# Kernel optimization log

Measured on AMD Instinct MI355X. Metric: run time of the kernel, lower is better.

## Reference

```python
import jax, jax.numpy as jnp
import numpy as np

B, T, C = 2, 2048, 2048
H = 16
D = C // H  # head_size = 128
ROPE_BASE = 10000.0


def _rope_cos_sin(seq_len, dim, dtype=jnp.float32):
    # torchtune RotaryPositionalEmbeddings: interleaved pair rotation
    inv_freq = 1.0 / (ROPE_BASE ** (jnp.arange(0, dim, 2, dtype=jnp.float32) / dim))  # [D/2]
    ang = jnp.arange(seq_len, dtype=jnp.float32)[:, None] * inv_freq[None, :]  # [T, D/2]
    return jnp.cos(ang).astype(dtype), jnp.sin(ang).astype(dtype)


def _apply_rope(x, cos, sin):
    # x: [B, T, H, D]; rotate interleaved pairs (even, odd)
    x1 = x[..., 0::2]
    x2 = x[..., 1::2]
    c = cos[None, :, None, :]
    s = sin[None, :, None, :]
    out = jnp.stack([x1 * c - x2 * s, x1 * s + x2 * c], axis=-1)  # [B,T,H,D/2,2]
    return out.reshape(x.shape)


def setup_inputs() -> dict:
    key = jax.random.key(0)
    ks = jax.random.split(key, 5)
    scale = 1.0 / np.sqrt(C)
    return {
        "x": jax.random.normal(ks[0], (B, T, C), jnp.float32),
        "W_attn": jax.random.normal(ks[1], (C, 3 * C), jnp.float32) * scale,
        "b_attn": jax.random.normal(ks[2], (3 * C,), jnp.float32) * 0.01,
        "W_proj": jax.random.normal(ks[3], (C, C), jnp.float32) * scale,
        "b_proj": jax.random.normal(ks[4], (C,), jnp.float32) * 0.01,
    }


def reference(x, W_attn, b_attn, W_proj, b_proj):
    b, t, c = x.shape
    qkv = x @ W_attn + b_attn                      # [B,T,3C]
    q, k, v = jnp.split(qkv, 3, axis=-1)
    q = q.reshape(b, t, H, D)
    k = k.reshape(b, t, H, D)
    v = v.reshape(b, t, H, D)
    cos, sin = _rope_cos_sin(t, D, x.dtype)
    q = _apply_rope(q, cos, sin)
    k = _apply_rope(k, cos, sin)
    # [B,H,T,D]
    q = q.transpose(0, 2, 1, 3)
    k = k.transpose(0, 2, 1, 3)
    v = v.transpose(0, 2, 1, 3)
    scores = jnp.einsum("bhqd,bhkd->bhqk", q, k) / jnp.sqrt(jnp.asarray(D, x.dtype))
    causal = jnp.tril(jnp.ones((t, t), dtype=bool))  # [T,T]
    scores = jnp.where(causal[None, None], scores, jnp.asarray(-jnp.inf, scores.dtype))
    probs = jax.nn.softmax(scores, axis=-1)
    out = jnp.einsum("bhqk,bhkd->bhqd", probs, v)  # [B,H,T,D]
    out = out.transpose(0, 2, 1, 3).reshape(b, t, c)
    return out @ W_proj + b_proj
```

## Files before the change

### kernel.cpp

```cpp
#include <hip/hip_runtime.h>
#include <hip/hip_bf16.h>
#include <math.h>

#define B_ 2
#define T_ 2048
#define C_ 2048
#define H_ 16
#define D_ 128
#define M_ (B_ * T_)
#define N3C (3 * C_)

typedef __attribute__((ext_vector_type(8))) short v8s;
typedef __attribute__((ext_vector_type(4))) float v4f;

typedef const __attribute__((address_space(1))) void* gas_t;
typedef __attribute__((address_space(3))) void* las_t;

__device__ __forceinline__ void gl16(const void* g, void* l) {
  __builtin_amdgcn_global_load_lds((gas_t)g, (las_t)l, 16, 0, 0);
}
__device__ __forceinline__ v8s ldv(const unsigned short* p) { return *(const v8s*)p; }

__device__ inline unsigned short f2bf(float f) {
  unsigned u = __builtin_bit_cast(unsigned, f);
  u += 0x7FFFu + ((u >> 16) & 1u);
  return (unsigned short)(u >> 16);
}
__device__ inline float bf2f(unsigned short h) {
  unsigned u = (unsigned)h << 16;
  return __builtin_bit_cast(float, u);
}

__global__ __launch_bounds__(256) void rope_tab(float2* __restrict__ tab) {
  const int i = blockIdx.x * 256 + threadIdx.x;
  const int t = i >> 6;
  const int ip = i & 63;
  const float RC = 13.28771237954945f / 64.0f;
  float inv = exp2f(-(float)ip * RC);
  float s, c;
  sincosf((float)t * inv, &s, &c);
  float2 v; v.x = c; v.y = s;
  tab[i] = v;
}

__global__ __launch_bounds__(256) void split_rows(
    const float* __restrict__ X, unsigned short* __restrict__ XH,
    unsigned short* __restrict__ XL) {
  const long i4 = ((long)blockIdx.x * 256 + threadIdx.x) * 4;
  float4 v = *(const float4*)(X + i4);
  ushort4 hh, ll;
  hh.x = f2bf(v.x); ll.x = f2bf(v.x - bf2f(hh.x));
  hh.y = f2bf(v.y); ll.y = f2bf(v.y - bf2f(hh.y));
  hh.z = f2bf(v.z); ll.z = f2bf(v.z - bf2f(hh.z));
  hh.w = f2bf(v.w); ll.w = f2bf(v.w - bf2f(hh.w));
  *(ushort4*)&XH[i4] = hh;
  *(ushort4*)&XL[i4] = ll;
}

__global__ __launch_bounds__(256) void convert_wT(
    const float* __restrict__ W, unsigned short* __restrict__ WH,
    unsigned short* __restrict__ WL, int K, int N) {
  __shared__ float Ts[64][68];
  const int tid = threadIdx.x;
  const int n0 = blockIdx.x * 64;
  const int k0 = blockIdx.y * 64;
#pragma unroll
  for (int it = 0; it < 4; ++it) {
    int f = it * 256 + tid;
    int r = f >> 4;
    int c4 = (f & 15) * 4;
    float4 v = *(const float4*)(W + (long)(k0 + r) * N + n0 + c4);
    *(float4*)&Ts[r][c4] = v;
  }
  __syncthreads();
#pragma unroll
  for (int it = 0; it < 4; ++it) {
    int f = it * 256 + tid;
    int rn = f >> 4;
    int c4 = (f & 15) * 4;
    float x0 = Ts[c4 + 0][rn];
    float x1 = Ts[c4 + 1][rn];
    float x2 = Ts[c4 + 2][rn];
    float x3 = Ts[c4 + 3][rn];
    ushort4 hh, ll;
    hh.x = f2bf(x0); ll.x = f2bf(x0 - bf2f(hh.x));
    hh.y = f2bf(x1); ll.y = f2bf(x1 - bf2f(hh.y));
    hh.z = f2bf(x2); ll.z = f2bf(x2 - bf2f(hh.z));
    hh.w = f2bf(x3); ll.w = f2bf(x3 - bf2f(hh.w));
    long o = (long)(n0 + rn) * K + k0 + c4;
    *(ushort4*)&WH[o] = hh;
    *(ushort4*)&WL[o] = ll;
  }
}

#define BAR() do { asm volatile("" ::: "memory"); __builtin_amdgcn_s_barrier(); asm volatile("" ::: "memory"); } while (0)

__global__ __launch_bounds__(512, 1) void gemm_proj_2g(
    const unsigned short* __restrict__ AH, const unsigned short* __restrict__ AL,
    const unsigned short* __restrict__ BH, const unsigned short* __restrict__ BL,
    const float* __restrict__ bias, float* __restrict__ C, int K, int N) {
  __shared__ unsigned short smem[2 * 24576];

  const int tid = threadIdx.x;
  const int lane = tid & 63;
  const int w = tid >> 6;
  const int lm = lane & 15;
  const int quad = lane >> 4;

  const int gx = gridDim.x;
  const int lin = blockIdx.y * gx + blockIdx.x;
  const int pid_m = (lin & 7) + ((lin >> 3) / gx) * 8;
  const int pid_n = (lin >> 3) % gx;
  const int bm = pid_m * 256;
  const int bn = pid_n * 128;

  const int wm = (w & 1) * 128;
  const int wn = (w >> 1) * 32;

  const unsigned short* aS[4]; int aD[4];
  {
    const int seg = tid >> 8;
    const int rr = (tid & 255) >> 2;
    const int cc = tid & 3;
#pragma unroll
    for (int j = 0; j < 4; ++j) {
      int row = (j >> 1) * 64 + seg * 128 + rr;
      int pl = j & 1;
      int c = cc ^ ((row >> 1) & 3);
      aS[j] = (pl ? AL : AH) + (size_t)(bm + row) * K + c * 8;
      aD[j] = pl * 8192 + row * 32 + cc * 8;
    }
  }
  const unsigned short* bS[2]; int bD[2];
#pragma unroll
  for (int j = 0; j < 2; ++j) {
    int p = tid;
    int row = p >> 2;
    int c = (p & 3) ^ ((row >> 1) & 3);
    bS[j] = (j ? BL : BH) + (size_t)(bn + row) * K + c * 8;
    bD[j] = 16384 + j * 4096 + p * 8;
  }

  v4f acc[8][2];
#pragma unroll
  for (int i = 0; i < 8; ++i)
#pragma unroll
    for (int j = 0; j < 2; ++j) {
      v4f z = {0.f, 0.f, 0.f, 0.f};
      acc[i][j] = z;
    }

  const int kswz = (quad ^ ((lm >> 1) & 3)) * 8;
  const int nk = K >> 5;

  gl16(bS[0], smem + bD[0]);
  gl16(bS[1], smem + bD[1]);
  gl16(aS[0], smem + aD[0]);
  gl16(aS[1], smem + aD[1]);
  gl16(aS[2], smem + aD[2]);
  gl16(aS[3], smem + aD[3]);

#define MM3(MT, NT, AH_, AL_)                                                           \
  acc[MT][NT] = __builtin_amdgcn_mfma_f32_16x16x32_bf16(AH_, bh##NT, acc[MT][NT], 0, 0, 0); \
  acc[MT][NT] = __builtin_amdgcn_mfma_f32_16x16x32_bf16(AH_, bl##NT, acc[MT][NT], 0, 0, 0); \
  acc[MT][NT] = __builtin_amdgcn_mfma_f32_16x16x32_bf16(AL_, bh##NT, acc[MT][NT], 0, 0, 0);
#define MROW(MT, XH_, XL_) MM3(MT, 0, XH_, XL_) MM3(MT, 1, XH_, XL_)
#define AFRAG(MT) ldv(sbuf + (wm + (MT) * 16 + lm) * 32 + kswz)
#define AFRAGL(MT) ldv(sbuf + 8192 + (wm + (MT) * 16 + lm) * 32 + kswz)

  for (int t = 0; t < nk; ++t) {
    const unsigned short* sbuf = smem + (t & 1) * 24576;
    unsigned short* nbuf = (unsigned short*)smem + ((t + 1) & 1) * 24576;
    const int kn = (t + 1) * 32;
    const bool pf = (t + 1 < nk);

    if (pf) {
      gl16(bS[0] + kn, nbuf + bD[0]);
      gl16(bS[1] + kn, nbuf + bD[1]);
      asm volatile("s_waitcnt vmcnt(4)" ::: "memory");
    } else {
      asm volatile("s_waitcnt vmcnt(2)" ::: "memory");
    }
    BAR();

    v8s bh0 = ldv(sbuf + 16384 + (wn + lm) * 32 + kswz);
    v8s bl0 = ldv(sbuf + 20480 + (wn + lm) * 32 + kswz);
    v8s bh1 = ldv(sbuf + 16384 + (wn + 16 + lm) * 32 + kswz);
    v8s bl1 = ldv(sbuf + 20480 + (wn + 16 + lm) * 32 + kswz);
    {
      v8s x0h = AFRAG(0), x0l = AFRAGL(0);
      v8s x1h = AFRAG(1), x1l = AFRAGL(1);
      v8s x2h = AFRAG(2), x2l = AFRAGL(2);
      v8s x3h = AFRAG(3), x3l = AFRAGL(3);
      __builtin_amdgcn_s_setprio(1);
      MROW(0, x0h, x0l)
      MROW(1, x1h, x1l)
      __builtin_amdgcn_s_setprio(0);
      if (pf) {
        gl16(aS[0] + kn, nbuf + aD[0]);
        gl16(aS[1] + kn, nbuf + aD[1]);
      }
      __builtin_amdgcn_s_setprio(1);
      MROW(2, x2h, x2l)
      MROW(3, x3h, x3l)
      __builtin_amdgcn_s_setprio(0);
    }

    if (pf) {
      gl16(aS[2] + kn, nbuf + aD[2]);
      gl16(aS[3] + kn, nbuf + aD[3]);
      asm volatile("s_waitcnt vmcnt(6)" ::: "memory");
    } else {
      asm volatile("s_waitcnt vmcnt(0)" ::: "memory");
    }
    BAR();

    {
      v8s x4h = AFRAG(4), x4l = AFRAGL(4);
      v8s x5h = AFRAG(5), x5l = AFRAGL(5);
      v8s x6h = AFRAG(6), x6l = AFRAGL(6);
      v8s x7h = AFRAG(7), x7l = AFRAGL(7);
      __builtin_amdgcn_s_setprio(1);
      MROW(4, x4h, x4l)
      MROW(5, x5h, x5l)
      MROW(6, x6h, x6l)
      MROW(7, x7h, x7l)
      __builtin_amdgcn_s_setprio(0);
    }
    BAR();
  }
#undef AFRAGL
#undef AFRAG
#undef MROW
#undef MM3

  __syncthreads();
  float* eps = (float*)smem;
  float* myeps = eps + w * 1088;

  float bv[2];
#pragma unroll
  for (int nt = 0; nt < 2; ++nt) bv[nt] = bias[bn + wn + nt * 16 + lm];

  const int r2 = lane >> 2;
  const int c4 = (lane & 3) * 4;
#pragma unroll
  for (int mt = 0; mt < 8; ++mt) {
#pragma unroll
    for (int nt = 0; nt < 2; ++nt)
#pragma unroll
      for (int r = 0; r < 4; ++r)
        myeps[(quad * 4 + r) * 68 + nt * 16 + lm] = acc[mt][nt][r] + bv[nt];
    float* dst = C + (size_t)(bm + wm + mt * 16 + r2) * N + bn + wn + c4;
#pragma unroll
    for (int i = 0; i < 2; ++i) {
      float4 v = *(float4*)&myeps[r2 * 68 + c4 + i * 16];
      *(float4*)&dst[i * 16] = v;
    }
  }
}

__global__ __launch_bounds__(512, 2) void gemm_qkv_8ph(
    const unsigned short* __restrict__ AH, const unsigned short* __restrict__ AL,
    const unsigned short* __restrict__ BH, const unsigned short* __restrict__ BL,
    const float* __restrict__ bias, const float2* __restrict__ tab,
    unsigned short* __restrict__ QH, unsigned short* __restrict__ QL,
    unsigned short* __restrict__ KH, unsigned short* __restrict__ KL,
    unsigned short* __restrict__ VH, unsigned short* __restrict__ VL,
    int K, int N) {
  __shared__ unsigned short smem[2 * 28672];

  const int tid = threadIdx.x;
  const int lane = tid & 63;
  const int w = tid >> 6;
  const int lm = lane & 15;
  const int quad = lane >> 4;

  const int gx = gridDim.x;
  const int lin = blockIdx.y * gx + blockIdx.x;
  const int pid_m = (lin & 7) + ((lin >> 3) / gx) * 8;
  const int pid_n = (lin >> 3) % gx;
  const int bm = pid_m * 256;
  const int bn = pid_n * 192;

  const int wm = (w & 1) * 128;
  const int wn = (w >> 1) * 48;

  const unsigned short* aS[4]; int aD[4];
  {
    const int seg = tid >> 8;
    const int rr = (tid & 255) >> 2;
    const int cc = tid & 3;
#pragma unroll
    for (int j = 0; j < 4; ++j) {
      int row = (j >> 1) * 64 + seg * 128 + rr;
      int pl = j & 1;
      int c = cc ^ ((row >> 1) & 3);
      aS[j] = (pl ? AL : AH) + (size_t)(bm + row) * K + c * 8;
      aD[j] = pl * 8192 + row * 32 + cc * 8;
    }
  }
  const unsigned short* bS[3]; int bD[3];
#pragma unroll
  for (int j = 0; j < 3; ++j) {
    int g = tid + 512 * j;
    int pl = (g >= 768) ? 1 : 0;
    int p = g - pl * 768;
    int row = p >> 2;
    int c = (p & 3) ^ ((row >> 1) & 3);
    bS[j] = (pl ? BL : BH) + (size_t)(bn + row) * K + c * 8;
    bD[j] = 16384 + pl * 6144 + p * 8;
  }

  v4f acc[8][3];
#pragma unroll
  for (int i = 0; i < 8; ++i)
#pragma unroll
    for (int j = 0; j < 3; ++j) {
      v4f z = {0.f, 0.f, 0.f, 0.f};
      acc[i][j] = z;
    }

  const int kswz = (quad ^ ((lm >> 1) & 3)) * 8;
  const int nk = K >> 5;

  gl16(bS[0], smem + bD[0]);
  gl16(bS[1], smem + bD[1]);
  gl16(bS[2], smem + bD[2]);
  gl16(aS[0], smem + aD[0]);
  gl16(aS[1], smem + aD[1]);
  gl16(aS[2], smem + aD[2]);
  gl16(aS[3], smem + aD[3]);

#define MM3(MT, NT, AH_, AL_)                                                           \
  acc[MT][NT] = __builtin_amdgcn_mfma_f32_16x16x32_bf16(AH_, bh##NT, acc[MT][NT], 0, 0, 0); \
  acc[MT][NT] = __builtin_amdgcn_mfma_f32_16x16x32_bf16(AH_, bl##NT, acc[MT][NT], 0, 0, 0); \
  acc[MT][NT] = __builtin_amdgcn_mfma_f32_16x16x32_bf16(AL_, bh##NT, acc[MT][NT], 0, 0, 0);
#define MROW(MT, XH_, XL_) MM3(MT, 0, XH_, XL_) MM3(MT, 1, XH_, XL_) MM3(MT, 2, XH_, XL_)
#define AFRAG(MT) ldv(sbuf + (wm + (MT) * 16 + lm) * 32 + kswz)
#define AFRAGL(MT) ldv(sbuf + 8192 + (wm + (MT) * 16 + lm) * 32 + kswz)

  for (int t = 0; t < nk; ++t) {
    const unsigned short* sbuf = smem + (t & 1) * 28672;
    unsigned short* nbuf = (unsigned short*)smem + ((t + 1) & 1) * 28672;
    const int kn = (t + 1) * 32;
    const bool pf = (t + 1 < nk);

    if (pf) {
      gl16(bS[0] + kn, nbuf + bD[0]);
      gl16(bS[1] + kn, nbuf + bD[1]);
      gl16(bS[2] + kn, nbuf + bD[2]);
      asm volatile("s_waitcnt vmcnt(5)" ::: "memory");
    } else {
      asm volatile("s_waitcnt vmcnt(2)" ::: "memory");
    }
    BAR();

    v8s bh0 = ldv(sbuf + 16384 + (wn + lm) * 32 + kswz);
    v8s bl0 = ldv(sbuf + 22528 + (wn + lm) * 32 + kswz);
    v8s bh1 = ldv(sbuf + 16384 + (wn + 16 + lm) * 32 + kswz);
    v8s bl1 = ldv(sbuf + 22528 + (wn + 16 + lm) * 32 + kswz);
    v8s bh2 = ldv(sbuf + 16384 + (wn + 32 + lm) * 32 + kswz);
    v8s bl2 = ldv(sbuf + 22528 + (wn + 32 + lm) * 32 + kswz);
    {
      v8s x0h = AFRAG(0), x0l = AFRAGL(0);
      v8s x1h = AFRAG(1), x1l = AFRAGL(1);
      v8s x2h = AFRAG(2), x2l = AFRAGL(2);
      v8s x3h = AFRAG(3), x3l = AFRAGL(3);
      __builtin_amdgcn_s_setprio(1);
      MROW(0, x0h, x0l)
      MROW(1, x1h, x1l)
      __builtin_amdgcn_s_setprio(0);
      if (pf) {
        gl16(aS[0] + kn, nbuf + aD[0]);
        gl16(aS[1] + kn, nbuf + aD[1]);
      }
      __builtin_amdgcn_s_setprio(1);
      MROW(2, x2h, x2l)
      MROW(3, x3h, x3l)
      __builtin_amdgcn_s_setprio(0);
    }

    if (pf) {
      gl16(aS[2] + kn, nbuf + aD[2]);
      gl16(aS[3] + kn, nbuf + aD[3]);
      asm volatile("s_waitcnt vmcnt(7)" ::: "memory");
    } else {
      asm volatile("s_waitcnt vmcnt(0)" ::: "memory");
    }
    BAR();

    {
      v8s x4h = AFRAG(4), x4l = AFRAGL(4);
      v8s x5h = AFRAG(5), x5l = AFRAGL(5);
      v8s x6h = AFRAG(6), x6l = AFRAGL(6);
      v8s x7h = AFRAG(7), x7l = AFRAGL(7);
      __builtin_amdgcn_s_setprio(1);
      MROW(4, x4h, x4l)
      MROW(5, x5h, x5l)
      MROW(6, x6h, x6l)
      MROW(7, x7h, x7l)
      __builtin_amdgcn_s_setprio(0);
    }
    BAR();
  }
#undef AFRAGL
#undef AFRAG
#undef MROW
#undef MM3

  __syncthreads();
  float* eps = (float*)smem;
  float* myeps = eps + w * 1088;

  float bv[3];
#pragma unroll
  for (int nt = 0; nt < 3; ++nt) bv[nt] = bias[bn + wn + nt * 16 + lm];

  const int r2 = lane >> 2;
  const int c4 = (lane & 3) * 4;

#pragma unroll
  for (int mt = 0; mt < 8; ++mt) {
#pragma unroll
    for (int nt = 0; nt < 3; ++nt)
#pragma unroll
      for (int r = 0; r < 4; ++r)
        myeps[(quad * 4 + r) * 68 + nt * 16 + lm] = acc[mt][nt][r] + bv[nt];

    const int row = bm + wm + mt * 16 + r2;
    const int bb = row >> 11;
    const int tt = row & 2047;
#pragma unroll
    for (int i = 0; i < 3; ++i) {
      float4 v = *(float4*)&myeps[r2 * 68 + c4 + i * 16];
      const int col = bn + wn + c4 + i * 16;
      const int part = col >> 11;
      const int cc = col & 2047;
      const int hh = cc >> 7;
      const int d0 = cc & 127;
      size_t dst = ((size_t)(bb * H_ + hh) * T_ + tt) * D_ + d0;
      if (part < 2) {
        const float sc = part ? 1.0f : 0.12751879523595298f;
        const int ip = d0 >> 1;
        float2 t0 = tab[tt * 64 + ip];
        float2 t1 = tab[tt * 64 + ip + 1];
        float ox0 = (v.x * t0.x - v.y * t0.y) * sc;
        float oy0 = (v.x * t0.y + v.y * t0.x) * sc;
        float ox1 = (v.z * t1.x - v.w * t1.y) * sc;
        float oy1 = (v.z * t1.y + v.w * t1.x) * sc;
        unsigned short h0 = f2bf(ox0), h1 = f2bf(oy0);
        unsigned short h2 = f2bf(ox1), h3 = f2bf(oy1);
        ushort4 hv; hv.x = h0; hv.y = h1; hv.z = h2; hv.w = h3;
        ushort4 lv;
        lv.x = f2bf(ox0 - bf2f(h0)); lv.y = f2bf(oy0 - bf2f(h1));
        lv.z = f2bf(ox1 - bf2f(h2)); lv.w = f2bf(oy1 - bf2f(h3));
        unsigned short* OH = part ? KH : QH;
        unsigned short* OL = part ? KL : QL;
        *(ushort4*)&OH[dst] = hv;
        *(ushort4*)&OL[dst] = lv;
      } else {
        unsigned short h0 = f2bf(v.x), h1 = f2bf(v.y);
        unsigned short h2 = f2bf(v.z), h3 = f2bf(v.w);
        ushort4 hv; hv.x = h0; hv.y = h1; hv.z = h2; hv.w = h3;
        ushort4 lv;
        lv.x = f2bf(v.x - bf2f(h0)); lv.y = f2bf(v.y - bf2f(h1));
        lv.z = f2bf(v.z - bf2f(h2)); lv.w = f2bf(v.w - bf2f(h3));
        *(ushort4*)&VH[dst] = hv;
        *(ushort4*)&VL[dst] = lv;
      }
    }
  }
}

__global__ __launch_bounds__(256) void v_trans(
    const unsigned short* __restrict__ VH, const unsigned short* __restrict__ VL,
    unsigned short* __restrict__ VTH, unsigned short* __restrict__ VTL) {
  const int tb = blockIdx.x;
  const int h = blockIdx.y;
  const int b = blockIdx.z;
  const int tid = threadIdx.x;

  __shared__ unsigned short TH[128][66];
  __shared__ unsigned short TL[128][66];

  const size_t base = (size_t)(b * H_ + h) * T_ * D_;
#pragma unroll
  for (int it = 0; it < 4; ++it) {
    int f = it * 256 + tid;
    int r = f >> 4;
    int c8 = (f & 15) * 8;
    uint4 hv = *(const uint4*)&VH[base + (size_t)(tb * 64 + r) * D_ + c8];
    uint4 lv = *(const uint4*)&VL[base + (size_t)(tb * 64 + r) * D_ + c8];
    const unsigned short* hp = (const unsigned short*)&hv;
    const unsigned short* lp = (const unsigned short*)&lv;
#pragma unroll
    for (int j = 0; j < 8; ++j) {
      TH[c8 + j][r] = hp[j];
      TL[c8 + j][r] = lp[j];
    }
  }
  __syncthreads();
  const size_t obase = (size_t)(b * H_ + h) * D_ * T_;
#pragma unroll
  for (int it = 0; it < 4; ++it) {
    int f = it * 256 + tid;
    int d = f >> 3;
    int c8 = (f & 7) * 8;
    unsigned short th[8], tl[8];
#pragma unroll
    for (int j = 0; j < 8; ++j) { th[j] = TH[d][c8 + j]; tl[j] = TL[d][c8 + j]; }
    size_t dst = obase + (size_t)d * T_ + tb * 64 + c8;
    *(uint4*)&VTH[dst] = *(uint4*)th;
    *(uint4*)&VTL[dst] = *(uint4*)tl;
  }
}

__global__ __launch_bounds__(512, 4) void attn_mfma(
    const unsigned short* __restrict__ QH, const unsigned short* __restrict__ QL,
    const unsigned short* __restrict__ KH, const unsigned short* __restrict__ KL,
    const unsigned short* __restrict__ VTH, const unsigned short* __restrict__ VTL,
    unsigned short* __restrict__ OHp, unsigned short* __restrict__ OLp) {
  const int qb = (int)gridDim.x - 1 - (int)blockIdx.x;
  const int h = blockIdx.y;
  const int b = blockIdx.z;
  const int tid = threadIdx.x;
  const int lane = tid & 63;
  const int w = tid >> 6;
  const int lm = lane & 15;
  const int quad = lane >> 4;

  __shared__ unsigned short KS_H[32][136], KS_L[32][136];
  __shared__ unsigned short VS_H[128][40], VS_L[128][40];
  __shared__ unsigned short PS_H[128][40], PS_L[128][40];

  const size_t qbase = ((size_t)(b * H_ + h) * T_ + qb * 128 + w * 16 + lm) * D_;
  v8s qh[4], ql[4];
#pragma unroll
  for (int ks = 0; ks < 4; ++ks) {
    qh[ks] = *(const v8s*)&QH[qbase + ks * 32 + quad * 8];
    ql[ks] = *(const v8s*)&QL[qbase + ks * 32 + quad * 8];
  }

  v8s ones;
#pragma unroll
  for (int j = 0; j < 8; ++j) ones[j] = (short)0x3F80;

  const int kr = tid >> 4;
  const int kc = (tid & 15) * 8;
  const int vd = tid >> 2;
  const int vc = (tid & 3) * 8;

  const size_t kbase0 = (size_t)(b * H_ + h) * T_ * D_;
  const size_t vbase0 = (size_t)(b * H_ + h) * D_ * T_;
  const int nkb = 4 * qb + 4;

  uint4 khp = *(const uint4*)&KH[kbase0 + (size_t)kr * D_ + kc];
  uint4 klp = *(const uint4*)&KL[kbase0 + (size_t)kr * D_ + kc];
  uint4 vhp = *(const uint4*)&VTH[vbase0 + (size_t)vd * T_ + vc];
  uint4 vlp = *(const uint4*)&VTL[vbase0 + (size_t)vd * T_ + vc];

  v4f acc_o[8], acc_l;
#pragma unroll
  for (int nt = 0; nt < 8; ++nt) {
    v4f z = {0.f, 0.f, 0.f, 0.f};
    acc_o[nt] = z;
  }
  {
    v4f z = {0.f, 0.f, 0.f, 0.f};
    acc_l = z;
  }

  const float M2 = 32.0f;

  for (int kb = 0; kb < nkb; ++kb) {
    __syncthreads();
    *(uint4*)&KS_H[kr][kc] = khp;
    *(uint4*)&KS_L[kr][kc] = klp;
    *(uint4*)&VS_H[vd][vc] = vhp;
    *(uint4*)&VS_L[vd][vc] = vlp;
    __syncthreads();

    if (kb + 1 < nkb) {
      size_t kg = kbase0 + (size_t)((kb + 1) * 32 + kr) * D_ + kc;
      khp = *(const uint4*)&KH[kg];
      klp = *(const uint4*)&KL[kg];
      size_t vg = vbase0 + (size_t)vd * T_ + (kb + 1) * 32 + vc;
      vhp = *(const uint4*)&VTH[vg];
      vlp = *(const uint4*)&VTL[vg];
    }

    v4f s0, s1;
    {
      v4f z = {0.f, 0.f, 0.f, 0.f};
      s0 = z; s1 = z;
    }
#pragma unroll
    for (int ks = 0; ks < 4; ++ks) {
      int k8 = ks * 32 + quad * 8;
      v8s bh0 = *(const v8s*)&KS_H[lm][k8];
      v8s bl0 = *(const v8s*)&KS_L[lm][k8];
      v8s bh1 = *(const v8s*)&KS_H[16 + lm][k8];
      v8s bl1 = *(const v8s*)&KS_L[16 + lm][k8];
      s0 = __builtin_amdgcn_mfma_f32_16x16x32_bf16(qh[ks], bh0, s0, 0, 0, 0);
      s1 = __builtin_amdgcn_mfma_f32_16x16x32_bf16(qh[ks], bh1, s1, 0, 0, 0);
      s0 = __builtin_amdgcn_mfma_f32_16x16x32_bf16(qh[ks], bl0, s0, 0, 0, 0);
      s1 = __builtin_amdgcn_mfma_f32_16x16x32_bf16(qh[ks], bl1, s1, 0, 0, 0);
      s0 = __builtin_amdgcn_mfma_f32_16x16x32_bf16(ql[ks], bh0, s0, 0, 0, 0);
      s1 = __builtin_amdgcn_mfma_f32_16x16x32_bf16(ql[ks], bh1, s1, 0, 0, 0);
    }

#pragma unroll
    for (int r = 0; r < 4; ++r) {
      int rowg = qb * 128 + w * 16 + quad * 4 + r;
      float v0 = (kb * 32 + lm > rowg) ? -INFINITY : s0[r];
      float v1 = (kb * 32 + 16 + lm > rowg) ? -INFINITY : s1[r];
      float p0 = __builtin_amdgcn_exp2f(v0 - M2);
      float p1 = __builtin_amdgcn_exp2f(v1 - M2);

      int prow = w * 16 + quad * 4 + r;
      unsigned short p0h = f2bf(p0);
      PS_H[prow][lm] = p0h;
      PS_L[prow][lm] = f2bf(p0 - bf2f(p0h));
      unsigned short p1h = f2bf(p1);
      PS_H[prow][16 + lm] = p1h;
      PS_L[prow][16 + lm] = f2bf(p1 - bf2f(p1h));
    }

    v8s ph = *(const v8s*)&PS_H[w * 16 + lm][quad * 8];
    v8s pl = *(const v8s*)&PS_L[w * 16 + lm][quad * 8];
    acc_l = __builtin_amdgcn_mfma_f32_16x16x32_bf16(ph, ones, acc_l, 0, 0, 0);
    acc_l = __builtin_amdgcn_mfma_f32_16x16x32_bf16(pl, ones, acc_l, 0, 0, 0);
#pragma unroll
    for (int nt = 0; nt < 8; ++nt) {
      v8s vh = *(const v8s*)&VS_H[nt * 16 + lm][quad * 8];
      v8s vl = *(const v8s*)&VS_L[nt * 16 + lm][quad * 8];
      acc_o[nt] = __builtin_amdgcn_mfma_f32_16x16x32_bf16(ph, vh, acc_o[nt], 0, 0, 0);
      acc_o[nt] = __builtin_amdgcn_mfma_f32_16x16x32_bf16(ph, vl, acc_o[nt], 0, 0, 0);
      acc_o[nt] = __builtin_amdgcn_mfma_f32_16x16x32_bf16(pl, vh, acc_o[nt], 0, 0, 0);
    }
  }

#pragma unroll
  for (int r = 0; r < 4; ++r) {
    float invl = 1.0f / acc_l[r];
    size_t row = (size_t)(b * T_ + qb * 128 + w * 16 + quad * 4 + r);
#pragma unroll
    for (int nt = 0; nt < 8; ++nt) {
      float o = acc_o[nt][r] * invl;
      unsigned short oh = f2bf(o);
      size_t idx = row * C_ + h * D_ + nt * 16 + lm;
      OHp[idx] = oh;
      OLp[idx] = f2bf(o - bf2f(oh));
    }
  }
}

extern "C" void kernel_launch(void* const* d_in, const int* in_sizes, int n_in,
                              void* d_out, int out_size, void* d_ws, size_t ws_size,
                              hipStream_t stream) {
  const float* x      = (const float*)d_in[0];
  const float* W_attn = (const float*)d_in[1];
  const float* b_attn = (const float*)d_in[2];
  const float* W_proj = (const float*)d_in[3];
  const float* b_proj = (const float*)d_in[4];
  float* out = (float*)d_out;

  char* wsb = (char*)d_ws;
  const size_t MiB = 1048576;
  unsigned short* XH   = (unsigned short*)(wsb + 0 * MiB);
  unsigned short* XL   = (unsigned short*)(wsb + 16 * MiB);
  unsigned short* WtaH = (unsigned short*)(wsb + 32 * MiB);
  unsigned short* WtaL = (unsigned short*)(wsb + 56 * MiB);
  unsigned short* QH   = (unsigned short*)(wsb + 80 * MiB);
  unsigned short* QL   = (unsigned short*)(wsb + 96 * MiB);
  unsigned short* KH   = (unsigned short*)(wsb + 112 * MiB);
  unsigned short* KL   = (unsigned short*)(wsb + 128 * MiB);
  unsigned short* VH   = (unsigned short*)(wsb + 144 * MiB);
  unsigned short* VL   = (unsigned short*)(wsb + 160 * MiB);
  float2*         tab  = (float2*)(wsb + 176 * MiB);
  unsigned short* VTH  = (unsigned short*)(wsb + 0 * MiB);
  unsigned short* VTL  = (unsigned short*)(wsb + 16 * MiB);
  unsigned short* WtpH = (unsigned short*)(wsb + 32 * MiB);
  unsigned short* WtpL = (unsigned short*)(wsb + 40 * MiB);
  unsigned short* AOH  = (unsigned short*)(wsb + 48 * MiB);
  unsigned short* AOL  = (unsigned short*)(wsb + 64 * MiB);

  rope_tab<<<dim3((T_ * 64) / 256), 256, 0, stream>>>(tab);
  convert_wT<<<dim3(N3C / 64, C_ / 64), 256, 0, stream>>>(W_attn, WtaH, WtaL, C_, N3C);
  split_rows<<<dim3((M_ * C_) / 1024), 256, 0, stream>>>(x, XH, XL);
  gemm_qkv_8ph<<<dim3(N3C / 192, M_ / 256), 512, 0, stream>>>(
      XH, XL, WtaH, WtaL, b_attn, tab, QH, QL, KH, KL, VH, VL, C_, N3C);
  v_trans<<<dim3(T_ / 64, H_, B_), 256, 0, stream>>>(VH, VL, VTH, VTL);
  convert_wT<<<dim3(C_ / 64, C_ / 64), 256, 0, stream>>>(W_proj, WtpH, WtpL, C_, C_);
  attn_mfma<<<dim3(T_ / 128, H_, B_), 512, 0, stream>>>(
      QH, QL, KH, KL, VTH, VTL, AOH, AOL);
  gemm_proj_2g<<<dim3(C_ / 128, M_ / 256), 512, 0, stream>>>(
      AOH, AOL, WtpH, WtpL, b_proj, out, C_, C_);
}
```

Measured before the change: 693.2 us.

## Give each attention wave two query row tiles and halve block threads

The attention kernel now launches 256 threads instead of 512, and each wave computes two 16-row query tiles instead of one. Each K/V fragment read from LDS is reused across both tiles, and every thread stages twice as many K/V elements per step. This cuts LDS read traffic and the number of waves per block, at the cost of more registers per thread (launch bounds drop to 256,2) and so possibly lower occupancy.

```diff
diff --git a/kernel.cpp b/kernel.cpp
--- a/kernel.cpp
+++ b/kernel.cpp
@@ -516,7 +516,7 @@
   }
 }
 
-__global__ __launch_bounds__(512, 4) void attn_mfma(
+__global__ __launch_bounds__(256, 2) void attn_mfma(
     const unsigned short* __restrict__ QH, const unsigned short* __restrict__ QL,
     const unsigned short* __restrict__ KH, const unsigned short* __restrict__ KL,
     const unsigned short* __restrict__ VTH, const unsigned short* __restrict__ VTL,
@@ -534,12 +534,16 @@
   __shared__ unsigned short VS_H[128][40], VS_L[128][40];
   __shared__ unsigned short PS_H[128][40], PS_L[128][40];
 
-  const size_t qbase = ((size_t)(b * H_ + h) * T_ + qb * 128 + w * 16 + lm) * D_;
-  v8s qh[4], ql[4];
-#pragma unroll
-  for (int ks = 0; ks < 4; ++ks) {
-    qh[ks] = *(const v8s*)&QH[qbase + ks * 32 + quad * 8];
-    ql[ks] = *(const v8s*)&QL[qbase + ks * 32 + quad * 8];
+  v8s qh[2][4], ql[2][4];
+#pragma unroll
+  for (int mq = 0; mq < 2; ++mq) {
+    const size_t qbase =
+        ((size_t)(b * H_ + h) * T_ + qb * 128 + w * 32 + mq * 16 + lm) * D_;
+#pragma unroll
+    for (int ks = 0; ks < 4; ++ks) {
+      qh[mq][ks] = *(const v8s*)&QH[qbase + ks * 32 + quad * 8];
+      ql[mq][ks] = *(const v8s*)&QL[qbase + ks * 32 + quad * 8];
+    }
   }
 
   v8s ones;
@@ -555,45 +559,59 @@
   const size_t vbase0 = (size_t)(b * H_ + h) * D_ * T_;
   const int nkb = 4 * qb + 4;
 
-  uint4 khp = *(const uint4*)&KH[kbase0 + (size_t)kr * D_ + kc];
-  uint4 klp = *(const uint4*)&KL[kbase0 + (size_t)kr * D_ + kc];
-  uint4 vhp = *(const uint4*)&VTH[vbase0 + (size_t)vd * T_ + vc];
-  uint4 vlp = *(const uint4*)&VTL[vbase0 + (size_t)vd * T_ + vc];
-
-  v4f acc_o[8], acc_l;
-#pragma unroll
-  for (int nt = 0; nt < 8; ++nt) {
+  uint4 khp0 = *(const uint4*)&KH[kbase0 + (size_t)kr * D_ + kc];
+  uint4 khp1 = *(const uint4*)&KH[kbase0 + (size_t)(kr + 16) * D_ + kc];
+  uint4 klp0 = *(const uint4*)&KL[kbase0 + (size_t)kr * D_ + kc];
+  uint4 klp1 = *(const uint4*)&KL[kbase0 + (size_t)(kr + 16) * D_ + kc];
+  uint4 vhp0 = *(const uint4*)&VTH[vbase0 + (size_t)vd * T_ + vc];
+  uint4 vhp1 = *(const uint4*)&VTH[vbase0 + (size_t)(vd + 64) * T_ + vc];
+  uint4 vlp0 = *(const uint4*)&VTL[vbase0 + (size_t)vd * T_ + vc];
+  uint4 vlp1 = *(const uint4*)&VTL[vbase0 + (size_t)(vd + 64) * T_ + vc];
+
+  v4f acc_o[2][8], acc_l[2];
+#pragma unroll
+  for (int mq = 0; mq < 2; ++mq) {
+#pragma unroll
+    for (int nt = 0; nt < 8; ++nt) {
+      v4f z = {0.f, 0.f, 0.f, 0.f};
+      acc_o[mq][nt] = z;
+    }
     v4f z = {0.f, 0.f, 0.f, 0.f};
-    acc_o[nt] = z;
-  }
-  {
-    v4f z = {0.f, 0.f, 0.f, 0.f};
-    acc_l = z;
+    acc_l[mq] = z;
   }
 
   const float M2 = 32.0f;
 
   for (int kb = 0; kb < nkb; ++kb) {
     __syncthreads();
-    *(uint4*)&KS_H[kr][kc] = khp;
-    *(uint4*)&KS_L[kr][kc] = klp;
-    *(uint4*)&VS_H[vd][vc] = vhp;
-    *(uint4*)&VS_L[vd][vc] = vlp;
+    *(uint4*)&KS_H[kr][kc] = khp0;
+    *(uint4*)&KS_H[kr + 16][kc] = khp1;
+    *(uint4*)&KS_L[kr][kc] = klp0;
+    *(uint4*)&KS_L[kr + 16][kc] = klp1;
+    *(uint4*)&VS_H[vd][vc] = vhp0;
+    *(uint4*)&VS_H[vd + 64][vc] = vhp1;
+    *(uint4*)&VS_L[vd][vc] = vlp0;
+    *(uint4*)&VS_L[vd + 64][vc] = vlp1;
     __syncthreads();
 
     if (kb + 1 < nkb) {
       size_t kg = kbase0 + (size_t)((kb + 1) * 32 + kr) * D_ + kc;
-      khp = *(const uint4*)&KH[kg];
-      klp = *(const uint4*)&KL[kg];
+      khp0 = *(const uint4*)&KH[kg];
+      khp1 = *(const uint4*)&KH[kg + (size_t)16 * D_];
+      klp0 = *(const uint4*)&KL[kg];
+      klp1 = *(const uint4*)&KL[kg + (size_t)16 * D_];
       size_t vg = vbase0 + (size_t)vd * T_ + (kb + 1) * 32 + vc;
-      vhp = *(const uint4*)&VTH[vg];
-      vlp = *(const uint4*)&VTL[vg];
-    }
-
-    v4f s0, s1;
-    {
+      vhp0 = *(const uint4*)&VTH[vg];
+      vhp1 = *(const uint4*)&VTH[vg + (size_t)64 * T_];
+      vlp0 = *(const uint4*)&VTL[vg];
+      vlp1 = *(const uint4*)&VTL[vg + (size_t)64 * T_];
+    }
+
+    v4f s[2][2];
+#pragma unroll
+    for (int mq = 0; mq < 2; ++mq) {
       v4f z = {0.f, 0.f, 0.f, 0.f};
-      s0 = z; s1 = z;
+      s[mq][0] = z; s[mq][1] = z;
     }
 #pragma unroll
     for (int ks = 0; ks < 4; ++ks) {
@@ -602,56 +620,72 @@
       v8s bl0 = *(const v8s*)&KS_L[lm][k8];
       v8s bh1 = *(const v8s*)&KS_H[16 + lm][k8];
       v8s bl1 = *(const v8s*)&KS_L[16 + lm][k8];
-      s0 = __builtin_amdgcn_mfma_f32_16x16x32_bf16(qh[ks], bh0, s0, 0, 0, 0);
-      s1 = __builtin_amdgcn_mfma_f32_16x16x32_bf16(qh[ks], bh1, s1, 0, 0, 0);
-      s0 = __builtin_amdgcn_mfma_f32_16x16x32_bf16(qh[ks], bl0, s0, 0, 0, 0);
-      s1 = __builtin_amdgcn_mfma_f32_16x16x32_bf16(qh[ks], bl1, s1, 0, 0, 0);
-      s0 = __builtin_amdgcn_mfma_f32_16x16x32_bf16(ql[ks], bh0, s0, 0, 0, 0);
-      s1 = __builtin_amdgcn_mfma_f32_16x16x32_bf16(ql[ks], bh1, s1, 0, 0, 0);
-    }
-
-#pragma unroll
-    for (int r = 0; r < 4; ++r) {
-      int rowg = qb * 128 + w * 16 + quad * 4 + r;
-      float v0 = (kb * 32 + lm > rowg) ? -INFINITY : s0[r];
-      float v1 = (kb * 32 + 16 + lm > rowg) ? -INFINITY : s1[r];
-      float p0 = __builtin_amdgcn_exp2f(v0 - M2);
-      float p1 = __builtin_amdgcn_exp2f(v1 - M2);
-
-      int prow = w * 16 + quad * 4 + r;
-      unsigned short p0h = f2bf(p0);
-      PS_H[prow][lm] = p0h;
-      PS_L[prow][lm] = f2bf(p0 - bf2f(p0h));
-      unsigned short p1h = f2bf(p1);
-      PS_H[prow][16 + lm] = p1h;
-      PS_L[prow][16 + lm] = f2bf(p1 - bf2f(p1h));
-    }
-
-    v8s ph = *(const v8s*)&PS_H[w * 16 + lm][quad * 8];
-    v8s pl = *(const v8s*)&PS_L[w * 16 + lm][quad * 8];
-    acc_l = __builtin_amdgcn_mfma_f32_16x16x32_bf16(ph, ones, acc_l, 0, 0, 0);
-    acc_l = __builtin_amdgcn_mfma_f32_16x16x32_bf16(pl, ones, acc_l, 0, 0, 0);
+#pragma unroll
+      for (int mq = 0; mq < 2; ++mq) {
+        s[mq][0] = __builtin_amdgcn_mfma_f32_16x16x32_bf16(qh[mq][ks], bh0, s[mq][0], 0, 0, 0);
+        s[mq][1] = __builtin_amdgcn_mfma_f32_16x16x32_bf16(qh[mq][ks], bh1, s[mq][1], 0, 0, 0);
+        s[mq][0] = __builtin_amdgcn_mfma_f32_16x16x32_bf16(qh[mq][ks], bl0, s[mq][0], 0, 0, 0);
+        s[mq][1] = __builtin_amdgcn_mfma_f32_16x16x32_bf16(qh[mq][ks], bl1, s[mq][1], 0, 0, 0);
+        s[mq][0] = __builtin_amdgcn_mfma_f32_16x16x32_bf16(ql[mq][ks], bh0, s[mq][0], 0, 0, 0);
+        s[mq][1] = __builtin_amdgcn_mfma_f32_16x16x32_bf16(ql[mq][ks], bh1, s[mq][1], 0, 0, 0);
+      }
+    }
+
+#pragma unroll
+    for (int mq = 0; mq < 2; ++mq) {
+#pragma unroll
+      for (int r = 0; r < 4; ++r) {
+        int rowg = qb * 128 + w * 32 + mq * 16 + quad * 4 + r;
+        float v0 = (kb * 32 + lm > rowg) ? -INFINITY : s[mq][0][r];
+        float v1 = (kb * 32 + 16 + lm > rowg) ? -INFINITY : s[mq][1][r];
+        float p0 = __builtin_amdgcn_exp2f(v0 - M2);
+        float p1 = __builtin_amdgcn_exp2f(v1 - M2);
+
+        int prow = w * 32 + mq * 16 + quad * 4 + r;
+        unsigned short p0h = f2bf(p0);
+        PS_H[prow][lm] = p0h;
+        PS_L[prow][lm] = f2bf(p0 - bf2f(p0h));
+        unsigned short p1h = f2bf(p1);
+        PS_H[prow][16 + lm] = p1h;
+        PS_L[prow][16 + lm] = f2bf(p1 - bf2f(p1h));
+      }
+    }
+
+    v8s ph0 = *(const v8s*)&PS_H[w * 32 + lm][quad * 8];
+    v8s pl0 = *(const v8s*)&PS_L[w * 32 + lm][quad * 8];
+    v8s ph1 = *(const v8s*)&PS_H[w * 32 + 16 + lm][quad * 8];
+    v8s pl1 = *(const v8s*)&PS_L[w * 32 + 16 + lm][quad * 8];
+    acc_l[0] = __builtin_amdgcn_mfma_f32_16x16x32_bf16(ph0, ones, acc_l[0], 0, 0, 0);
+    acc_l[0] = __builtin_amdgcn_mfma_f32_16x16x32_bf16(pl0, ones, acc_l[0], 0, 0, 0);
+    acc_l[1] = __builtin_amdgcn_mfma_f32_16x16x32_bf16(ph1, ones, acc_l[1], 0, 0, 0);
+    acc_l[1] = __builtin_amdgcn_mfma_f32_16x16x32_bf16(pl1, ones, acc_l[1], 0, 0, 0);
 #pragma unroll
     for (int nt = 0; nt < 8; ++nt) {
       v8s vh = *(const v8s*)&VS_H[nt * 16 + lm][quad * 8];
       v8s vl = *(const v8s*)&VS_L[nt * 16 + lm][quad * 8];
-      acc_o[nt] = __builtin_amdgcn_mfma_f32_16x16x32_bf16(ph, vh, acc_o[nt], 0, 0, 0);
-      acc_o[nt] = __builtin_amdgcn_mfma_f32_16x16x32_bf16(ph, vl, acc_o[nt], 0, 0, 0);
-      acc_o[nt] = __builtin_amdgcn_mfma_f32_16x16x32_bf16(pl, vh, acc_o[nt], 0, 0, 0);
-    }
-  }
-
-#pragma unroll
-  for (int r = 0; r < 4; ++r) {
-    float invl = 1.0f / acc_l[r];
-    size_t row = (size_t)(b * T_ + qb * 128 + w * 16 + quad * 4 + r);
-#pragma unroll
-    for (int nt = 0; nt < 8; ++nt) {
-      float o = acc_o[nt][r] * invl;
-      unsigned short oh = f2bf(o);
-      size_t idx = row * C_ + h * D_ + nt * 16 + lm;
-      OHp[idx] = oh;
-      OLp[idx] = f2bf(o - bf2f(oh));
+      acc_o[0][nt] = __builtin_amdgcn_mfma_f32_16x16x32_bf16(ph0, vh, acc_o[0][nt], 0, 0, 0);
+      acc_o[0][nt] = __builtin_amdgcn_mfma_f32_16x16x32_bf16(ph0, vl, acc_o[0][nt], 0, 0, 0);
+      acc_o[0][nt] = __builtin_amdgcn_mfma_f32_16x16x32_bf16(pl0, vh, acc_o[0][nt], 0, 0, 0);
+      acc_o[1][nt] = __builtin_amdgcn_mfma_f32_16x16x32_bf16(ph1, vh, acc_o[1][nt], 0, 0, 0);
+      acc_o[1][nt] = __builtin_amdgcn_mfma_f32_16x16x32_bf16(ph1, vl, acc_o[1][nt], 0, 0, 0);
+      acc_o[1][nt] = __builtin_amdgcn_mfma_f32_16x16x32_bf16(pl1, vh, acc_o[1][nt], 0, 0, 0);
+    }
+  }
+
+#pragma unroll
+  for (int mq = 0; mq < 2; ++mq) {
+#pragma unroll
+    for (int r = 0; r < 4; ++r) {
+      float invl = 1.0f / acc_l[mq][r];
+      size_t row = (size_t)(b * T_ + qb * 128 + w * 32 + mq * 16 + quad * 4 + r);
+#pragma unroll
+      for (int nt = 0; nt < 8; ++nt) {
+        float o = acc_o[mq][nt][r] * invl;
+        unsigned short oh = f2bf(o);
+        size_t idx = row * C_ + h * D_ + nt * 16 + lm;
+        OHp[idx] = oh;
+        OLp[idx] = f2bf(o - bf2f(oh));
+      }
     }
   }
 }
@@ -693,7 +727,7 @@
       XH, XL, WtaH, WtaL, b_attn, tab, QH, QL, KH, KL, VH, VL, C_, N3C);
   v_trans<<<dim3(T_ / 64, H_, B_), 256, 0, stream>>>(VH, VL, VTH, VTL);
   convert_wT<<<dim3(C_ / 64, C_ / 64), 256, 0, stream>>>(W_proj, WtpH, WtpL, C_, C_);
-  attn_mfma<<<dim3(T_ / 128, H_, B_), 512, 0, stream>>>(
+  attn_mfma<<<dim3(T_ / 128, H_, B_), 256, 0, stream>>>(
       QH, QL, KH, KL, VTH, VTL, AOH, AOL);
   gemm_proj_2g<<<dim3(C_ / 128, M_ / 256), 512, 0, stream>>>(
       AOH, AOL, WtpH, WtpL, b_proj, out, C_, C_);
```

Result: faster. 676.4 us (-2.4%).
